# Kernel optimization log

Measured on AMD Instinct MI355X. Metric: run time of the kernel, lower is better.

## Reference

```python
import jax, jax.numpy as jnp
import numpy as np

D_MODEL = 1024
NUM_HEADS = 16
NEG_INF = jnp.float32(-(2.0 ** 32) + 1.0)  # matches TF's -2**32+1 padding value


def setup_inputs() -> dict:
    key = jax.random.key(0)
    ks = jax.random.split(key, 10)
    B, S, D = 4, 1024, D_MODEL
    s = 1.0 / np.sqrt(D)
    return {
        "q": jax.random.normal(ks[0], (B, S, D), jnp.float32),
        "k": jax.random.normal(ks[1], (B, S, D), jnp.float32),
        "v": jax.random.normal(ks[2], (B, S, D), jnp.float32),
        "mask": jax.random.randint(ks[3], (NUM_HEADS * B, 1, S), 0, 2, jnp.int32),
        "Wq": jax.random.normal(ks[4], (D, D), jnp.float32) * s,
        "bq": jnp.zeros((D,), jnp.float32),
        "Wk": jax.random.normal(ks[5], (D, D), jnp.float32) * s,
        "bk": jnp.zeros((D,), jnp.float32),
        "Wv": jax.random.normal(ks[6], (D, D), jnp.float32) * s,
        "bv": jnp.zeros((D,), jnp.float32),
    }


def _split_heads(x, h):
    # TF: concat(split(x, h, axis=2), axis=0) -> head index leading on batch dim
    B, S, D = x.shape
    dh = D // h
    return x.reshape(B, S, h, dh).transpose(2, 0, 1, 3).reshape(h * B, S, dh)


def _merge_heads(x, h):
    hB, S, dh = x.shape
    B = hB // h
    return x.reshape(h, B, S, dh).transpose(1, 2, 0, 3).reshape(B, S, h * dh)


def reference(q, k, v, mask, Wq, bq, Wk, bk, Wv, bv):
    h = NUM_HEADS
    qp = q @ Wq + bq
    kp = k @ Wk + bk
    vp = v @ Wv + bv
    qh = _split_heads(qp, h)  # [h*B, S, dh]
    kh = _split_heads(kp, h)
    vh = _split_heads(vp, h)
    dh = kh.shape[-1]
    logits = jnp.einsum('bqd,bkd->bqk', qh, kh) / jnp.sqrt(jnp.float32(dh))
    logits = jnp.where(mask == 0, NEG_INF, logits)  # padding mask, broadcast [h*B,1,S]
    S = qh.shape[1]
    causal = jnp.tril(jnp.ones((S, S), jnp.bool_))
    logits = jnp.where(causal[None], logits, NEG_INF)
    attn = jax.nn.softmax(logits, axis=-1)
    out = jnp.einsum('bqk,bkd->bqd', attn, vh)
    return _merge_heads(out, h)  # [B, S, d_model]
```

## Files before the change

kernel.cpp:

```cpp
#include <hip/hip_runtime.h>
#include <stdint.h>

#define DEV __device__ __forceinline__

typedef __attribute__((ext_vector_type(4))) float f32x4;
typedef __attribute__((ext_vector_type(8))) __bf16 bf16x8;
typedef __attribute__((ext_vector_type(8))) unsigned short ushort8;

DEV unsigned short f2bf(float f) {
    union { float f; unsigned int u; } v; v.f = f;
    unsigned int r = v.u + 0x7FFFu + ((v.u >> 16) & 1u);
    return (unsigned short)(r >> 16);
}
DEV float bf2f(unsigned short u) {
    union { unsigned int u; float f; } v; v.u = ((unsigned int)u) << 16;
    return v.f;
}
DEV int swz(int o) { return o ^ ((o >> 3) & 0x70); }

DEV void gload_lds16(const void* gptr, void* lptr) {
    __builtin_amdgcn_global_load_lds(
        (const __attribute__((address_space(1))) unsigned int*)gptr,
        (__attribute__((address_space(3))) unsigned int*)lptr, 16, 0, 0);
}

__global__ void k_convert(const float* __restrict__ q, const float* __restrict__ k,
                          const float* __restrict__ v, unsigned short* __restrict__ qb,
                          unsigned short* __restrict__ kb, unsigned short* __restrict__ vb) {
    const int z = blockIdx.z;
    const float* src = z == 0 ? q : (z == 1 ? k : v);
    unsigned short* dst = z == 0 ? qb : (z == 1 ? kb : vb);
    const size_t idx = ((size_t)blockIdx.x * 256 + threadIdx.x) * 8;
    f32x4 a = *(const f32x4*)(src + idx);
    f32x4 b = *(const f32x4*)(src + idx + 4);
    ushort8 o;
    o[0] = f2bf(a[0]); o[1] = f2bf(a[1]); o[2] = f2bf(a[2]); o[3] = f2bf(a[3]);
    o[4] = f2bf(b[0]); o[5] = f2bf(b[1]); o[6] = f2bf(b[2]); o[7] = f2bf(b[3]);
    *(ushort8*)(dst + idx) = o;
}

__global__ void k_convw(const float* __restrict__ Wq, const float* __restrict__ Wk,
                        const float* __restrict__ Wv, unsigned short* __restrict__ wt) {
    __shared__ float tile[64 * 65];
    const int z = blockIdx.z;
    const float* W = z == 0 ? Wq : (z == 1 ? Wk : Wv);
    unsigned short* dst = wt + (size_t)z * 1048576;
    const int k0 = blockIdx.x * 64, n0 = blockIdx.y * 64;
    const int t = threadIdx.x;
#pragma unroll
    for (int i = 0; i < 4; i++) {
        const int idx = i * 256 + t;
        const int row = idx >> 4, c4 = (idx & 15) * 4;
        f32x4 val = *(const f32x4*)(W + (size_t)(k0 + row) * 1024 + n0 + c4);
#pragma unroll
        for (int j = 0; j < 4; j++) tile[row * 65 + c4 + j] = val[j];
    }
    __syncthreads();
#pragma unroll
    for (int i = 0; i < 2; i++) {
        const int idx = i * 256 + t;
        const int nrow = idx >> 3, c8 = (idx & 7) * 8;
        ushort8 o;
#pragma unroll
        for (int j = 0; j < 8; j++) o[j] = f2bf(tile[(c8 + j) * 65 + nrow]);
        *(ushort8*)(dst + (size_t)(n0 + nrow) * 1024 + k0 + c8) = o;
    }
}

__global__ __launch_bounds__(256) void k_proj(
    const unsigned short* __restrict__ qb, const unsigned short* __restrict__ kb,
    const unsigned short* __restrict__ vb, const unsigned short* __restrict__ wt,
    const float* __restrict__ bq, const float* __restrict__ bk, const float* __restrict__ bv,
    unsigned short* __restrict__ qh, unsigned short* __restrict__ kh,
    unsigned short* __restrict__ vh) {
    const int z = blockIdx.z;
    const unsigned short* A  = z == 0 ? qb : (z == 1 ? kb : vb);
    const unsigned short* Bt = wt + (size_t)z * 1048576;
    const float* bias = z == 0 ? bq : (z == 1 ? bk : bv);
    unsigned short* outp = z == 0 ? qh : (z == 1 ? kh : vh);
    const float scale = z == 0 ? 0.125f : 1.0f;

    __shared__ unsigned short sA[128 * 64];
    __shared__ unsigned short sB[128 * 64];

    const int tid = threadIdx.x;
    const int w = tid >> 6, lane = tid & 63;
    const int c = lane & 15, gq = lane >> 4;
    const int wrow = w >> 1, wcol = w & 1;
    const int m0 = blockIdx.y * 128, n0 = blockIdx.x * 128;
    const int lr = lane >> 3;
    const int lcs = ((lane & 7) ^ (lane >> 3)) * 8;

    f32x4 acc[4][4] = {};

    for (int kt = 0; kt < 16; kt++) {
        __syncthreads();
        const int kb0 = kt * 64;
#pragma unroll
        for (int i = 0; i < 4; i++) {
            const int rbase = w * 32 + i * 8;
            gload_lds16(A  + (size_t)(m0 + rbase + lr) * 1024 + kb0 + lcs,
                        (char*)sA + rbase * 128);
            gload_lds16(Bt + (size_t)(n0 + rbase + lr) * 1024 + kb0 + lcs,
                        (char*)sB + rbase * 128);
        }
        __syncthreads();
#pragma unroll
        for (int kk = 0; kk < 2; kk++) {
            bf16x8 af[4], bfr[4];
#pragma unroll
            for (int i = 0; i < 4; i++) {
                af[i]  = *(const bf16x8*)((char*)sA +
                          swz((wrow * 64 + i * 16 + c) * 128 + kk * 64 + gq * 16));
                bfr[i] = *(const bf16x8*)((char*)sB +
                          swz((wcol * 64 + i * 16 + c) * 128 + kk * 64 + gq * 16));
            }
#pragma unroll
            for (int mi = 0; mi < 4; mi++)
#pragma unroll
                for (int ni = 0; ni < 4; ni++)
                    acc[mi][ni] = __builtin_amdgcn_mfma_f32_16x16x32_bf16(
                        af[mi], bfr[ni], acc[mi][ni], 0, 0, 0);
        }
    }

    float bvals[4];
#pragma unroll
    for (int ni = 0; ni < 4; ni++) bvals[ni] = bias[n0 + wcol * 64 + ni * 16 + c];

#pragma unroll
    for (int mi = 0; mi < 4; mi++)
#pragma unroll
        for (int ni = 0; ni < 4; ni++) {
            const int n = n0 + wcol * 64 + ni * 16 + c;
            const int head = n >> 6, d = n & 63;
#pragma unroll
            for (int r = 0; r < 4; r++) {
                const int m = m0 + wrow * 64 + mi * 16 + gq * 4 + r;
                const int bb = m >> 10, s = m & 1023;
                const float val = (acc[mi][ni][r] + bvals[ni]) * scale;
                outp[(size_t)((head << 2) + bb) * 65536 + (size_t)s * 64 + d] = f2bf(val);
            }
        }
}

__global__ void k_trv(const unsigned short* __restrict__ vh, unsigned short* __restrict__ vt) {
    __shared__ unsigned int tile[64 * 65];
    const int hb = blockIdx.y, s0 = blockIdx.x * 64;
    const int t = threadIdx.x;
#pragma unroll
    for (int it = 0; it < 2; it++) {
        const int idx = it * 256 + t;
        const int row = idx >> 3, c8 = (idx & 7) * 8;
        ushort8 val = *(const ushort8*)(vh + (size_t)hb * 65536 + (size_t)(s0 + row) * 64 + c8);
#pragma unroll
        for (int j = 0; j < 8; j++) tile[row * 65 + c8 + j] = val[j];
    }
    __syncthreads();
#pragma unroll
    for (int it = 0; it < 2; it++) {
        const int idx = it * 256 + t;
        const int d = idx >> 3, s8 = (idx & 7) * 8;
        ushort8 o;
#pragma unroll
        for (int j = 0; j < 8; j++) o[j] = (unsigned short)tile[(s8 + j) * 65 + d];
        *(ushort8*)(vt + (size_t)hb * 65536 + (size_t)d * 1024 + s0 + s8) = o;
    }
}

__global__ void k_vmean(const unsigned short* __restrict__ vt, float* __restrict__ vmean) {
    __shared__ float red[256];
    const int hb = blockIdx.x, t = threadIdx.x;
    const int d = t >> 2, part = t & 3;
    const unsigned short* p = vt + (size_t)hb * 65536 + (size_t)d * 1024 + part * 256;
    float sum = 0.f;
#pragma unroll 4
    for (int i = 0; i < 32; i++) {
        ushort8 v8 = *(const ushort8*)(p + i * 8);
#pragma unroll
        for (int j = 0; j < 8; j++) sum += bf2f(v8[j]);
    }
    red[t] = sum;
    __syncthreads();
    if (part == 0)
        vmean[hb * 64 + d] = (red[t] + red[t + 1] + red[t + 2] + red[t + 3]) * (1.0f / 1024.0f);
}

__global__ __launch_bounds__(256) void k_attn(
    const unsigned short* __restrict__ qh, const unsigned short* __restrict__ kh,
    const unsigned short* __restrict__ vt, const int* __restrict__ mask,
    const float* __restrict__ vmean, float* __restrict__ out) {
    __shared__ unsigned short sK[2][64 * 64];
    __shared__ unsigned short sV[2][64 * 64];
    __shared__ unsigned short sP[2][4 * 16 * 64];

    const int b = blockIdx.x, hb = blockIdx.y;
    const int tid = threadIdx.x;
    const int w = tid >> 6, lane = tid & 63;
    const int c = lane & 15, g = lane >> 4;
    const int qtA = b, qtB = 15 - b;
    const int tmax = qtB;
    const int q0A = qtA * 64 + w * 16, q0B = qtB * 64 + w * 16;
    const int bidx = hb & 3, head = hb >> 2;
    const size_t hboff = (size_t)hb * 65536;
    const int* mp = mask + hb * 1024;

    bf16x8 aqA[2], aqB[2];
#pragma unroll
    for (int kk = 0; kk < 2; kk++) {
        aqA[kk] = *(const bf16x8*)(qh + hboff + (size_t)(q0A + c) * 64 + kk * 32 + g * 8);
        aqB[kk] = *(const bf16x8*)(qh + hboff + (size_t)(q0B + c) * 64 + kk * 32 + g * 8);
    }

    f32x4 oaccA[4] = {}, oaccB[4] = {};
    float lsumA[4] = {0.f, 0.f, 0.f, 0.f}, lsumB[4] = {0.f, 0.f, 0.f, 0.f};
    float mrowA[4] = {-1e30f, -1e30f, -1e30f, -1e30f};
    float mrowB[4] = {-1e30f, -1e30f, -1e30f, -1e30f};

    const int srow = tid >> 3, sch = tid & 7;
    const int ssc = (sch ^ (srow & 7)) * 8;

    auto stage = [&](int t, int buf) {
        const int kv0 = t * 64;
#pragma unroll
        for (int i = 0; i < 2; i++) {
            const int row = i * 32 + srow;
            gload_lds16(kh + hboff + (size_t)(kv0 + row) * 64 + ssc,
                        (char*)sK[buf] + row * 128 + sch * 16);
        }
#pragma unroll
        for (int i = 0; i < 2; i++) {
            const int row = i * 32 + srow;
            gload_lds16(vt + hboff + (size_t)row * 1024 + kv0 + ssc,
                        (char*)sV[buf] + row * 128 + sch * 16);
        }
    };

    auto compute_tile = [&](int kv0, int q0, const bf16x8* aq, f32x4* oacc,
                            float* lsum, float* mrow, unsigned short* pw,
                            const unsigned short* sKc, const unsigned short* sVc) {
        f32x4 sacc[4] = {};
#pragma unroll
        for (int ns = 0; ns < 4; ns++) {
            const int kvl = ns * 16 + c;
#pragma unroll
            for (int kk = 0; kk < 2; kk++) {
                bf16x8 bk = *(const bf16x8*)((char*)sKc + swz(kvl * 128 + kk * 64 + g * 16));
                sacc[ns] = __builtin_amdgcn_mfma_f32_16x16x32_bf16(aq[kk], bk, sacc[ns], 0, 0, 0);
            }
        }
        float sv[4][4];
#pragma unroll
        for (int ns = 0; ns < 4; ns++) {
            const int kvg = kv0 + ns * 16 + c;
            const int mv = mp[kvg];
#pragma unroll
            for (int r = 0; r < 4; r++) {
                const int qg = q0 + g * 4 + r;
                sv[ns][r] = (mv != 0 && kvg <= qg) ? sacc[ns][r] : -1e30f;
            }
        }
#pragma unroll
        for (int r = 0; r < 4; r++) {
            float vmax = fmaxf(fmaxf(sv[0][r], sv[1][r]), fmaxf(sv[2][r], sv[3][r]));
            vmax = fmaxf(vmax, __shfl_xor(vmax, 1, 64));
            vmax = fmaxf(vmax, __shfl_xor(vmax, 2, 64));
            vmax = fmaxf(vmax, __shfl_xor(vmax, 4, 64));
            vmax = fmaxf(vmax, __shfl_xor(vmax, 8, 64));
            const float mnew = fmaxf(mrow[r], vmax);
            const float alpha = __expf(mrow[r] - mnew);
            mrow[r] = mnew;
            float rs = 0.f;
            const int ql = g * 4 + r;
#pragma unroll
            for (int ns = 0; ns < 4; ns++) {
                const float pv = __expf(sv[ns][r] - mnew);
                rs += pv;
                *(unsigned short*)((char*)pw + swz(ql * 128 + (ns * 16 + c) * 2)) = f2bf(pv);
            }
            rs += __shfl_xor(rs, 1, 64);
            rs += __shfl_xor(rs, 2, 64);
            rs += __shfl_xor(rs, 4, 64);
            rs += __shfl_xor(rs, 8, 64);
            lsum[r] = lsum[r] * alpha + rs;
#pragma unroll
            for (int nd = 0; nd < 4; nd++) oacc[nd][r] *= alpha;
        }
        asm volatile("s_waitcnt lgkmcnt(0)" ::: "memory");
#pragma unroll
        for (int ks = 0; ks < 2; ks++) {
            const bf16x8 ap = *(const bf16x8*)((char*)pw + swz(c * 128 + ks * 64 + g * 16));
#pragma unroll
            for (int nd = 0; nd < 4; nd++) {
                const int d = nd * 16 + c;
                const bf16x8 bv = *(const bf16x8*)((char*)sVc + swz(d * 128 + ks * 64 + g * 16));
                oacc[nd] = __builtin_amdgcn_mfma_f32_16x16x32_bf16(ap, bv, oacc[nd], 0, 0, 0);
            }
        }
    };

    stage(0, 0);
    for (int t = 0; t <= tmax; t++) {
        const int cur = t & 1;
        if (t < tmax) {
            stage(t + 1, cur ^ 1);
            asm volatile("s_waitcnt vmcnt(4)" ::: "memory");
        } else {
            asm volatile("s_waitcnt vmcnt(0)" ::: "memory");
        }
        __builtin_amdgcn_s_barrier();
        __builtin_amdgcn_sched_barrier(0);
        const int kv0 = t * 64;
        if (t <= qtA)
            compute_tile(kv0, q0A, aqA, oaccA, lsumA, mrowA,
                         sP[0] + w * 1024, sK[cur], sV[cur]);
        compute_tile(kv0, q0B, aqB, oaccB, lsumB, mrowB,
                     sP[1] + w * 1024, sK[cur], sV[cur]);
        __builtin_amdgcn_sched_barrier(0);
        __builtin_amdgcn_s_barrier();
        __builtin_amdgcn_sched_barrier(0);
    }

    auto write_out = [&](int q0, f32x4* oacc, float* lsum, float* mrow) {
#pragma unroll
        for (int nd = 0; nd < 4; nd++)
#pragma unroll
            for (int r = 0; r < 4; r++) {
                const int s = q0 + g * 4 + r;
                const int dcol = nd * 16 + c;
                const float val = (mrow[r] < -5e29f) ? vmean[hb * 64 + dcol]
                                                     : oacc[nd][r] / lsum[r];
                out[(size_t)bidx * 1048576 + (size_t)s * 1024 + head * 64 + dcol] = val;
            }
    };
    write_out(q0A, oaccA, lsumA, mrowA);
    write_out(q0B, oaccB, lsumB, mrowB);
}

extern "C" void kernel_launch(void* const* d_in, const int* in_sizes, int n_in,
                              void* d_out, int out_size, void* d_ws, size_t ws_size,
                              hipStream_t stream) {
    const float* q  = (const float*)d_in[0];
    const float* k  = (const float*)d_in[1];
    const float* v  = (const float*)d_in[2];
    const int* mask = (const int*)d_in[3];
    const float* Wq = (const float*)d_in[4];
    const float* bq = (const float*)d_in[5];
    const float* Wk = (const float*)d_in[6];
    const float* bk = (const float*)d_in[7];
    const float* Wv = (const float*)d_in[8];
    const float* bv = (const float*)d_in[9];
    float* out = (float*)d_out;

    unsigned short* qb = (unsigned short*)d_ws;
    unsigned short* kb = qb + 4194304;
    unsigned short* vb = kb + 4194304;
    unsigned short* wt = vb + 4194304;
    unsigned short* qh = wt + 3 * 1048576;
    unsigned short* kh = qh + 4194304;
    unsigned short* vh = kh + 4194304;
    unsigned short* vt = vh + 4194304;
    float* vmean = (float*)(vt + 4194304);

    k_convert<<<dim3(2048, 1, 3), 256, 0, stream>>>(q, k, v, qb, kb, vb);
    k_convw<<<dim3(16, 16, 3), 256, 0, stream>>>(Wq, Wk, Wv, wt);
    k_proj<<<dim3(8, 32, 3), 256, 0, stream>>>(qb, kb, vb, wt, bq, bk, bv, qh, kh, vh);
    k_trv<<<dim3(16, 64), 256, 0, stream>>>(vh, vt);
    k_vmean<<<64, 256, 0, stream>>>(vt, vmean);
    k_attn<<<dim3(8, 64), 256, 0, stream>>>(qh, kh, vt, mask, vmean, out);
}
```

Before: 220.9 us.

## Split causal attention KV range into chunks with separate combine kernel

Replaces the paired-query-tile load balancing in the attention kernel with a split-KV scheme. Each query tile's causal KV range is divided into chunks of up to four tiles, and each chunk runs in its own block, giving 40 blocks per head-batch instead of 8. Partial outputs and row max/sum are written as bf16 and float to a scratch buffer that reuses the input-conversion workspace, and a new combine kernel merges them. The change also folds log2(e) into the Q scale so exp2f replaces __expf, and computes the V column mean inside the transpose kernel with atomics instead of a separate kernel. This adds a memset, an extra launch, bf16 rounding of partial outputs, and extra partial-result traffic.

```diff
diff --git a/kernel.cpp b/kernel.cpp
--- a/kernel.cpp
+++ b/kernel.cpp
@@ -78,7 +78,7 @@
     const unsigned short* Bt = wt + (size_t)z * 1048576;
     const float* bias = z == 0 ? bq : (z == 1 ? bk : bv);
     unsigned short* outp = z == 0 ? qh : (z == 1 ? kh : vh);
-    const float scale = z == 0 ? 0.125f : 1.0f;
+    const float scale = z == 0 ? 0.18033688011112042f : 1.0f;
 
     __shared__ unsigned short sA[128 * 64];
     __shared__ unsigned short sB[128 * 64];
@@ -144,7 +144,8 @@
         }
 }
 
-__global__ void k_trv(const unsigned short* __restrict__ vh, unsigned short* __restrict__ vt) {
+__global__ void k_trv(const unsigned short* __restrict__ vh, unsigned short* __restrict__ vt,
+                      float* __restrict__ vmean) {
     __shared__ unsigned int tile[64 * 65];
     const int hb = blockIdx.y, s0 = blockIdx.x * 64;
     const int t = threadIdx.x;
@@ -166,56 +167,47 @@
         for (int j = 0; j < 8; j++) o[j] = (unsigned short)tile[(s8 + j) * 65 + d];
         *(ushort8*)(vt + (size_t)hb * 65536 + (size_t)d * 1024 + s0 + s8) = o;
     }
-}
-
-__global__ void k_vmean(const unsigned short* __restrict__ vt, float* __restrict__ vmean) {
-    __shared__ float red[256];
-    const int hb = blockIdx.x, t = threadIdx.x;
-    const int d = t >> 2, part = t & 3;
-    const unsigned short* p = vt + (size_t)hb * 65536 + (size_t)d * 1024 + part * 256;
-    float sum = 0.f;
-#pragma unroll 4
-    for (int i = 0; i < 32; i++) {
-        ushort8 v8 = *(const ushort8*)(p + i * 8);
-#pragma unroll
-        for (int j = 0; j < 8; j++) sum += bf2f(v8[j]);
-    }
-    red[t] = sum;
-    __syncthreads();
-    if (part == 0)
-        vmean[hb * 64 + d] = (red[t] + red[t + 1] + red[t + 2] + red[t + 3]) * (1.0f / 1024.0f);
+    if (t < 64) {
+        float sum = 0.f;
+        for (int s = 0; s < 64; s++) sum += bf2f((unsigned short)tile[s * 65 + t]);
+        atomicAdd(&vmean[hb * 64 + t], sum * (1.0f / 1024.0f));
+    }
 }
 
 __global__ __launch_bounds__(256) void k_attn(
     const unsigned short* __restrict__ qh, const unsigned short* __restrict__ kh,
     const unsigned short* __restrict__ vt, const int* __restrict__ mask,
-    const float* __restrict__ vmean, float* __restrict__ out) {
+    const float* __restrict__ vmean, float* __restrict__ out,
+    char* __restrict__ part) {
     __shared__ unsigned short sK[2][64 * 64];
     __shared__ unsigned short sV[2][64 * 64];
-    __shared__ unsigned short sP[2][4 * 16 * 64];
-
-    const int b = blockIdx.x, hb = blockIdx.y;
+    __shared__ unsigned short sP[4 * 16 * 64];
+
+    const int idx = blockIdx.x, hb = blockIdx.y;
+    int qt, ch, nch;
+    if (idx < 4)       { qt = idx;                 ch = 0;             nch = 1; }
+    else if (idx < 12) { qt = 4 + ((idx - 4) >> 1);  ch = (idx - 4) & 1;  nch = 2; }
+    else if (idx < 24) { int r = idx - 12; qt = 8 + r / 3; ch = r % 3;   nch = 3; }
+    else               { qt = 12 + ((idx - 24) >> 2); ch = (idx - 24) & 3; nch = 4; }
+    const int t0 = ch * 4;
+    const int t1 = min(t0 + 4, qt + 1);
+
     const int tid = threadIdx.x;
     const int w = tid >> 6, lane = tid & 63;
     const int c = lane & 15, g = lane >> 4;
-    const int qtA = b, qtB = 15 - b;
-    const int tmax = qtB;
-    const int q0A = qtA * 64 + w * 16, q0B = qtB * 64 + w * 16;
-    const int bidx = hb & 3, head = hb >> 2;
+    const int q0 = qt * 64 + w * 16;
     const size_t hboff = (size_t)hb * 65536;
     const int* mp = mask + hb * 1024;
 
-    bf16x8 aqA[2], aqB[2];
-#pragma unroll
-    for (int kk = 0; kk < 2; kk++) {
-        aqA[kk] = *(const bf16x8*)(qh + hboff + (size_t)(q0A + c) * 64 + kk * 32 + g * 8);
-        aqB[kk] = *(const bf16x8*)(qh + hboff + (size_t)(q0B + c) * 64 + kk * 32 + g * 8);
-    }
-
-    f32x4 oaccA[4] = {}, oaccB[4] = {};
-    float lsumA[4] = {0.f, 0.f, 0.f, 0.f}, lsumB[4] = {0.f, 0.f, 0.f, 0.f};
-    float mrowA[4] = {-1e30f, -1e30f, -1e30f, -1e30f};
-    float mrowB[4] = {-1e30f, -1e30f, -1e30f, -1e30f};
+    bf16x8 aq[2];
+#pragma unroll
+    for (int kk = 0; kk < 2; kk++)
+        aq[kk] = *(const bf16x8*)(qh + hboff + (size_t)(q0 + c) * 64 + kk * 32 + g * 8);
+
+    f32x4 oacc[4] = {};
+    float lsum[4] = {0.f, 0.f, 0.f, 0.f};
+    float mrow[4] = {-1e30f, -1e30f, -1e30f, -1e30f};
+    unsigned short* pw = sP + w * 1024;
 
     const int srow = tid >> 3, sch = tid & 7;
     const int ssc = (sch ^ (srow & 7)) * 8;
@@ -236,9 +228,23 @@
         }
     };
 
-    auto compute_tile = [&](int kv0, int q0, const bf16x8* aq, f32x4* oacc,
-                            float* lsum, float* mrow, unsigned short* pw,
-                            const unsigned short* sKc, const unsigned short* sVc) {
+    stage(t0, 0);
+    for (int t = t0; t < t1; t++) {
+        const int cur = (t - t0) & 1;
+        if (t + 1 < t1) {
+            stage(t + 1, cur ^ 1);
+            asm volatile("s_waitcnt vmcnt(4)" ::: "memory");
+        } else {
+            asm volatile("s_waitcnt vmcnt(0)" ::: "memory");
+        }
+        __builtin_amdgcn_s_barrier();
+        __builtin_amdgcn_sched_barrier(0);
+
+        const int kv0 = t * 64;
+        const bool diag = (t == qt);
+        const unsigned short* sKc = sK[cur];
+        const unsigned short* sVc = sV[cur];
+
         f32x4 sacc[4] = {};
 #pragma unroll
         for (int ns = 0; ns < 4; ns++) {
@@ -256,8 +262,8 @@
             const int mv = mp[kvg];
 #pragma unroll
             for (int r = 0; r < 4; r++) {
-                const int qg = q0 + g * 4 + r;
-                sv[ns][r] = (mv != 0 && kvg <= qg) ? sacc[ns][r] : -1e30f;
+                const bool ok = (mv != 0) && (!diag || kvg <= q0 + g * 4 + r);
+                sv[ns][r] = ok ? sacc[ns][r] : -1e30f;
             }
         }
 #pragma unroll
@@ -268,13 +274,13 @@
             vmax = fmaxf(vmax, __shfl_xor(vmax, 4, 64));
             vmax = fmaxf(vmax, __shfl_xor(vmax, 8, 64));
             const float mnew = fmaxf(mrow[r], vmax);
-            const float alpha = __expf(mrow[r] - mnew);
+            const float alpha = exp2f(mrow[r] - mnew);
             mrow[r] = mnew;
             float rs = 0.f;
             const int ql = g * 4 + r;
 #pragma unroll
             for (int ns = 0; ns < 4; ns++) {
-                const float pv = __expf(sv[ns][r] - mnew);
+                const float pv = exp2f(sv[ns][r] - mnew);
                 rs += pv;
                 *(unsigned short*)((char*)pw + swz(ql * 128 + (ns * 16 + c) * 2)) = f2bf(pv);
             }
@@ -293,35 +299,17 @@
 #pragma unroll
             for (int nd = 0; nd < 4; nd++) {
                 const int d = nd * 16 + c;
-                const bf16x8 bv = *(const bf16x8*)((char*)sVc + swz(d * 128 + ks * 64 + g * 16));
-                oacc[nd] = __builtin_amdgcn_mfma_f32_16x16x32_bf16(ap, bv, oacc[nd], 0, 0, 0);
-            }
-        }
-    };
-
-    stage(0, 0);
-    for (int t = 0; t <= tmax; t++) {
-        const int cur = t & 1;
-        if (t < tmax) {
-            stage(t + 1, cur ^ 1);
-            asm volatile("s_waitcnt vmcnt(4)" ::: "memory");
-        } else {
-            asm volatile("s_waitcnt vmcnt(0)" ::: "memory");
-        }
-        __builtin_amdgcn_s_barrier();
-        __builtin_amdgcn_sched_barrier(0);
-        const int kv0 = t * 64;
-        if (t <= qtA)
-            compute_tile(kv0, q0A, aqA, oaccA, lsumA, mrowA,
-                         sP[0] + w * 1024, sK[cur], sV[cur]);
-        compute_tile(kv0, q0B, aqB, oaccB, lsumB, mrowB,
-                     sP[1] + w * 1024, sK[cur], sV[cur]);
+                const bf16x8 bvv = *(const bf16x8*)((char*)sVc + swz(d * 128 + ks * 64 + g * 16));
+                oacc[nd] = __builtin_amdgcn_mfma_f32_16x16x32_bf16(ap, bvv, oacc[nd], 0, 0, 0);
+            }
+        }
         __builtin_amdgcn_sched_barrier(0);
         __builtin_amdgcn_s_barrier();
         __builtin_amdgcn_sched_barrier(0);
     }
 
-    auto write_out = [&](int q0, f32x4* oacc, float* lsum, float* mrow) {
+    if (nch == 1) {
+        const int bidx = hb & 3, head = hb >> 2;
 #pragma unroll
         for (int nd = 0; nd < 4; nd++)
 #pragma unroll
@@ -332,9 +320,77 @@
                                                      : oacc[nd][r] / lsum[r];
                 out[(size_t)bidx * 1048576 + (size_t)s * 1024 + head * 64 + dcol] = val;
             }
-    };
-    write_out(q0A, oaccA, lsumA, mrowA);
-    write_out(q0B, oaccB, lsumB, mrowB);
+    } else {
+        char* sp = part + ((size_t)hb * 36 + (idx - 4)) * 8704;
+        unsigned short* op = (unsigned short*)sp;
+#pragma unroll
+        for (int nd = 0; nd < 4; nd++)
+#pragma unroll
+            for (int r = 0; r < 4; r++)
+                op[(w * 16 + g * 4 + r) * 64 + nd * 16 + c] = f2bf(oacc[nd][r]);
+        if (c == 0) {
+            float* mo = (float*)(sp + 8192);
+            float* lo = (float*)(sp + 8448);
+#pragma unroll
+            for (int r = 0; r < 4; r++) {
+                mo[w * 16 + g * 4 + r] = mrow[r];
+                lo[w * 16 + g * 4 + r] = lsum[r];
+            }
+        }
+    }
+}
+
+__global__ __launch_bounds__(256) void k_combine(
+    const char* __restrict__ part, const float* __restrict__ vmean,
+    float* __restrict__ out) {
+    const int qt = 4 + blockIdx.x, hb = blockIdx.y;
+    int nch, base;
+    if (qt < 8)       { nch = 2; base = (qt - 4) * 2; }
+    else if (qt < 12) { nch = 3; base = 8 + (qt - 8) * 3; }
+    else              { nch = 4; base = 20 + (qt - 12) * 4; }
+    const int t = threadIdx.x;
+    const int row = t >> 2, d0 = (t & 3) * 16;
+    const char* sp0 = part + ((size_t)hb * 36 + base) * 8704;
+
+    float mi[4], li[4];
+    float m = -1e30f;
+#pragma unroll
+    for (int i = 0; i < 4; i++)
+        if (i < nch) {
+            const char* sp = sp0 + (size_t)i * 8704;
+            mi[i] = ((const float*)(sp + 8192))[row];
+            li[i] = ((const float*)(sp + 8448))[row];
+            m = fmaxf(m, mi[i]);
+        }
+    float L = 0.f;
+    float o[16];
+#pragma unroll
+    for (int j = 0; j < 16; j++) o[j] = 0.f;
+#pragma unroll
+    for (int i = 0; i < 4; i++)
+        if (i < nch) {
+            const float wgt = exp2f(mi[i] - m);
+            L += wgt * li[i];
+            const unsigned short* op =
+                (const unsigned short*)(sp0 + (size_t)i * 8704) + row * 64 + d0;
+            ushort8 a = *(const ushort8*)op;
+            ushort8 b = *(const ushort8*)(op + 8);
+#pragma unroll
+            for (int j = 0; j < 8; j++) {
+                o[j]     += wgt * bf2f(a[j]);
+                o[8 + j] += wgt * bf2f(b[j]);
+            }
+        }
+    const int bidx = hb & 3, head = hb >> 2;
+    float* dst = out + (size_t)bidx * 1048576 + (size_t)(qt * 64 + row) * 1024 + head * 64 + d0;
+    if (L > 0.f) {
+        const float inv = 1.0f / L;
+#pragma unroll
+        for (int j = 0; j < 16; j++) dst[j] = o[j] * inv;
+    } else {
+#pragma unroll
+        for (int j = 0; j < 16; j++) dst[j] = vmean[hb * 64 + d0 + j];
+    }
 }
 
 extern "C" void kernel_launch(void* const* d_in, const int* in_sizes, int n_in,
@@ -361,11 +417,13 @@
     unsigned short* vh = kh + 4194304;
     unsigned short* vt = vh + 4194304;
     float* vmean = (float*)(vt + 4194304);
+    char* part = (char*)qb;
 
     k_convert<<<dim3(2048, 1, 3), 256, 0, stream>>>(q, k, v, qb, kb, vb);
     k_convw<<<dim3(16, 16, 3), 256, 0, stream>>>(Wq, Wk, Wv, wt);
     k_proj<<<dim3(8, 32, 3), 256, 0, stream>>>(qb, kb, vb, wt, bq, bk, bv, qh, kh, vh);
-    k_trv<<<dim3(16, 64), 256, 0, stream>>>(vh, vt);
-    k_vmean<<<64, 256, 0, stream>>>(vt, vmean);
-    k_attn<<<dim3(8, 64), 256, 0, stream>>>(qh, kh, vt, mask, vmean, out);
-}
+    hipMemsetAsync(vmean, 0, 64 * 64 * sizeof(float), stream);
+    k_trv<<<dim3(16, 64), 256, 0, stream>>>(vh, vt, vmean);
+    k_attn<<<dim3(40, 64), 256, 0, stream>>>(qh, kh, vt, mask, vmean, out, part);
+    k_combine<<<dim3(12, 64), 256, 0, stream>>>(part, vmean, out);
+}
```

Result: no change. 222.1 us (+0.5%).
